# Optimization experiments

Hardware: AMD Instinct MI355X
Metric: run time of the kernel (lower is better)

The kernel has to match this reference:

```python
import jax, jax.numpy as jnp
import numpy as np

NUM_HEAD = 2
KR = 3          # kernel_range = [3, 3]
SHIFT = 1
N_P = KR * KR   # 9 taps
PAD = (KR // 2) * SHIFT  # 1
OFFSETS = [(i, j) for i in (-(KR // 2), 0, KR // 2) if True for j in ()]  # placeholder, real list below
OFFSETS = [(i, j) for i in range(-(KR // 2), KR // 2 + 1) for j in range(-(KR // 2), KR // 2 + 1)]


def _conv3x3(x, w, b):
    # x: [B,H,W,Cin], w: [3,3,Cin,Cout] -> SAME conv + bias
    y = jax.lax.conv_general_dilated(
        x, w, window_strides=(1, 1), padding='SAME',
        dimension_numbers=('NHWC', 'HWIO', 'NHWC'))
    return y + b


def setup_inputs() -> dict:
    key = jax.random.key(0)
    B, H, W, D = 4, 128, 128, 64
    ks = jax.random.split(key, 10)
    sc = 0.05  # small init like glorot
    return {
        'x': jax.random.normal(ks[0], (B, H, W, D), jnp.float32),
        # 1x1 conv kernels stored as matrices (equiv. to (1,1,Cin,Cout))
        'K_P': jax.random.normal(ks[1], (D, D * N_P), jnp.float32) * sc,
        'V_P': jax.random.normal(ks[2], (D, D * N_P), jnp.float32) * sc,
        'Q_P': jax.random.normal(ks[3], (D, D), jnp.float32) * sc,
        'ff1_kernel': jax.random.normal(ks[4], (D, D), jnp.float32) * sc,
        'ff1_bias': jax.random.normal(ks[5], (D,), jnp.float32) * sc,
        'ff2_kernel': jax.random.normal(ks[6], (3, 3, D, 2 * D), jnp.float32) * sc,
        'ff2_bias': jax.random.normal(ks[7], (2 * D,), jnp.float32) * sc,
        'ff3_kernel': jax.random.normal(ks[8], (3, 3, 2 * D, D), jnp.float32) * sc,
        'ff3_bias': jax.random.normal(ks[9], (D,), jnp.float32) * sc,
    }


def reference(x, K_P, V_P, Q_P, ff1_kernel, ff1_bias, ff2_kernel, ff2_bias,
              ff3_kernel, ff3_bias):
    B, H, W, D = x.shape
    hd = D // NUM_HEAD

    # 1x1 projections; K/V produce N_P channel chunks, one per tap
    x_k = jnp.einsum('bhwd,de->bhwe', x, K_P).reshape(B, H, W, N_P, D)
    x_v = jnp.einsum('bhwd,de->bhwe', x, V_P).reshape(B, H, W, N_P, D)
    x_q = jnp.einsum('bhwd,de->bhwe', x, Q_P)

    pad5 = ((0, 0), (PAD, PAD), (PAD, PAD), (0, 0), (0, 0))
    k_pad = jnp.pad(x_k, pad5)
    v_pad = jnp.pad(x_v, pad5)

    # tap t uses channel chunk t at spatial offset OFFSETS[t]*SHIFT
    def taps(padded):
        return jnp.stack(
            [padded[:, PAD + i * SHIFT:PAD + i * SHIFT + H,
                    PAD + j * SHIFT:PAD + j * SHIFT + W, t, :]
             for t, (i, j) in enumerate(OFFSETS)], axis=3)  # [B,H,W,N_P,D]

    k_taps = taps(k_pad)
    v_taps = taps(v_pad)

    # validity mask (padded taps get score 0 before softmax, as in original)
    m_pad = jnp.pad(jnp.ones((B, H, W), x.dtype), ((0, 0), (PAD, PAD), (PAD, PAD)))
    mask = jnp.stack(
        [m_pad[:, PAD + i * SHIFT:PAD + i * SHIFT + H,
               PAD + j * SHIFT:PAD + j * SHIFT + W]
         for (i, j) in OFFSETS], axis=3)  # [B,H,W,N_P]

    kh = k_taps.reshape(B, H, W, N_P, NUM_HEAD, hd)
    vh = v_taps.reshape(B, H, W, N_P, NUM_HEAD, hd)
    qh = x_q.reshape(B, H, W, NUM_HEAD, hd)

    # scores per head over taps; masked-multiply then /3, as in original
    scores = jnp.einsum('bhwtnc,bhwnc->bhwnt', kh, qh)
    scores = scores * mask[:, :, :, None, :] / 3.0
    alpha = jax.nn.softmax(scores, axis=-1)  # over taps
    attn = jnp.einsum('bhwnt,bhwtnc->bhwnc', alpha, vh).reshape(B, H, W, D)

    # FFN: 1x1 conv -> relu -> 3x3 conv -> relu -> 3x3 conv -> relu
    t = jax.nn.relu(jnp.einsum('bhwd,de->bhwe', attn, ff1_kernel) + ff1_bias)
    t = jax.nn.relu(_conv3x3(t, ff2_kernel, ff2_bias))
    t = jax.nn.relu(_conv3x3(t, ff3_kernel, ff3_bias))
    return t
```

## Files before the change

### kernel.cpp

```cpp
#include <hip/hip_runtime.h>


typedef _Float16 half8 __attribute__((ext_vector_type(8)));
typedef float f32x4 __attribute__((ext_vector_type(4)));

#define PLANE 524288

__device__ __forceinline__ f32x4 mfma16(half8 a, half8 b, f32x4 c) {
  return __builtin_amdgcn_mfma_f32_16x16x32_f16(a, b, c, 0, 0, 0);
}
__device__ __forceinline__ half8 ldfrag(const _Float16* p) { return *(const half8*)p; }
__device__ __forceinline__ half8 zfrag() { half8 z = {}; return z; }

__device__ __forceinline__ int xcd_swz(int n, int chunk) {
  return (n & 7) * chunk + (n >> 3);
}

__device__ __forceinline__ void gload_lds16(const _Float16* g, _Float16* l) {
  __builtin_amdgcn_global_load_lds(
      (const __attribute__((address_space(1))) void*)g,
      (__attribute__((address_space(3))) void*)l, 16, 0, 0);
}

__global__ __launch_bounds__(256) void prep(
    const float* __restrict__ x, const float* __restrict__ Kp,
    const float* __restrict__ Vp, const float* __restrict__ Qp,
    const float* __restrict__ W1, const float* __restrict__ F2,
    const float* __restrict__ F3, _Float16* __restrict__ xh,
    _Float16* __restrict__ out) {
  if (blockIdx.x < 2048) {
    const int b = xcd_swz(blockIdx.x, 256);
    const int t = threadIdx.x;
    const int px = b * 32 + (t >> 3);
    const int oct = t & 7;
    const float4* s = (const float4*)(x + (size_t)px * 64 + oct * 8);
    float4 a = s[0], b4 = s[1];
    half8 h = { (_Float16)a.x, (_Float16)a.y, (_Float16)a.z, (_Float16)a.w,
                (_Float16)b4.x, (_Float16)b4.y, (_Float16)b4.z, (_Float16)b4.w };
    *(half8*)(xh + (size_t)oct * PLANE + (size_t)px * 8) = h;
    return;
  }
  int e = (blockIdx.x - 2048) * 256 + threadIdx.x;
  int j = e & 7, l = (e >> 3) & 63, f = e >> 9;
  int l15 = l & 15, q8 = (l >> 4) * 8;
  float v;
  if (f < 8)        { int mb = f >> 1, kb = f & 1;
                      v = Qp[(kb*32 + q8 + j) * 64 + mb*16 + l15]; }
  else if (f < 80)  { int g = f - 8, t = g >> 3, mb = (g >> 1) & 3, kb = g & 1;
                      v = Kp[(kb*32 + q8 + j) * 576 + t*64 + mb*16 + l15]; }
  else if (f < 152) { int g = f - 80, t = g >> 3, kb = (g >> 2) & 1, nb = g & 3;
                      v = Vp[(kb*32 + q8 + j) * 576 + t*64 + nb*16 + l15]; }
  else if (f < 160) { int g = f - 152, kb = g >> 2, nb = g & 3;
                      v = W1[(kb*32 + q8 + j) * 64 + nb*16 + l15]; }
  else if (f < 304) { int g = f - 160, t = g >> 4, kb = (g >> 3) & 1, nb = g & 7;
                      v = F2[(t*64 + kb*32 + q8 + j) * 128 + nb*16 + l15]; }
  else              { int g = f - 304, t = g >> 4, kb = (g >> 2) & 3, nb = g & 3;
                      v = F3[(t*128 + kb*32 + q8 + j) * 64 + nb*16 + l15]; }
  out[e] = (_Float16)v;
}

__global__ __launch_bounds__(1024, 4) void attn_ff1(
    const _Float16* __restrict__ xh, const _Float16* __restrict__ wf,
    const float* __restrict__ f1b, _Float16* __restrict__ t1g) {
  extern __shared__ _Float16 smem[];
  const int lane = threadIdx.x & 63, wid = threadIdx.x >> 6;
  const int l15 = lane & 15, q8 = (lane >> 4) * 8;
  const int bid = xcd_swz(blockIdx.x, 32);
  const int row = bid * 2 + (wid >> 3);
  const int rw = wid & 7;
  const int p0 = row * 128 + rw * 16;
  const int h = row & 127;
  const int w0 = rw * 16;
  const int oct0 = lane >> 4;
  float* dent = (float*)(smem + 77824) + wid * 32;

  {
    for (int i = 0; i < 10; ++i) {
      int f = wid * 10 + i;
      if (f < 152)
        gload_lds16(wf + 4096 + (size_t)f * 512 + lane * 8,
                    smem + (size_t)f * 512);
    }
  }

  half8 ax0, ax1;
  {
    const size_t px = (size_t)(p0 + l15);
    ax0 = ldfrag(xh + (size_t)oct0 * PLANE + px * 8);
    ax1 = ldfrag(xh + (size_t)(oct0 + 4) * PLANE + px * 8);
  }
  f32x4 qT[4];
#pragma unroll
  for (int cb = 0; cb < 4; ++cb) {
    half8 aq0 = ldfrag(wf + (cb * 2 + 0) * 512 + lane * 8);
    half8 aq1 = ldfrag(wf + (cb * 2 + 1) * 512 + lane * 8);
    f32x4 c = {};
    c = mfma16(aq0, ax0, c);
    c = mfma16(aq1, ax1, c);
    qT[cb] = c;
  }

  auto load_tap = [&](int t, half8& x0, half8& x1) {
    const int dh = t / 3 - 1, dw = t % 3 - 1;
    const bool rk = (unsigned)(h + dh) < 128u;
    const bool cv = rk && ((unsigned)(w0 + l15 + dw) < 128u);
    const size_t px = (size_t)(p0 + l15 + dh * 128 + dw);
    x0 = cv ? ldfrag(xh + (size_t)oct0 * PLANE + px * 8) : zfrag();
    x1 = cv ? ldfrag(xh + (size_t)(oct0 + 4) * PLANE + px * 8) : zfrag();
  };

  float den0 = 0.f, den1 = 0.f;
  auto score_tap = [&](int t, half8& x0, half8& x1, float& e0, float& e1) {
    const int dh = t / 3 - 1;
    const bool rowok = (unsigned)(h + dh) < 128u;
    half8 kf[8];
    if (rowok) {
#pragma unroll
      for (int f = 0; f < 8; ++f)
        kf[f] = ldfrag(smem + (t * 8 + f) * 512 + lane * 8);
    }
    float pa = 0.f, pb = 0.f;
    if (rowok) {
#pragma unroll
      for (int cb = 0; cb < 4; ++cb) {
        f32x4 c = {};
        c = mfma16(kf[cb * 2 + 0], x0, c);
        c = mfma16(kf[cb * 2 + 1], x1, c);
        float d = qT[cb].x * c.x + qT[cb].y * c.y
                + qT[cb].z * c.z + qT[cb].w * c.w;
        if (cb < 2) pa += d; else pb += d;
      }
      pa += __shfl_xor(pa, 16, 64); pa += __shfl_xor(pa, 32, 64);
      pb += __shfl_xor(pb, 16, 64); pb += __shfl_xor(pb, 32, 64);
    }
    e0 = __expf(pa * (1.f / 3.f));
    e1 = __expf(pb * (1.f / 3.f));
    den0 += e0; den1 += e1;
  };

  half8 q0[3], q1[3];
  load_tap(0, q0[0], q1[0]);
  load_tap(1, q0[1], q1[1]);

  __syncthreads();

  float e0c, e1c;
  score_tap(0, q0[0], q1[0], e0c, e1c);

  const _Float16* BVl = smem + 36864;
  f32x4 at[4];
#pragma unroll
  for (int nb = 0; nb < 4; ++nb) at[nb] = f32x4{};

#pragma unroll
  for (int t = 0; t < 9; ++t) {
    if (t + 2 < 9) load_tap(t + 2, q0[(t + 2) % 3], q1[(t + 2) % 3]);
    const bool rowok = (unsigned)(h + (t / 3 - 1)) < 128u;
    if (rowok) {
      half8 vf[8];
#pragma unroll
      for (int f = 0; f < 8; ++f)
        vf[f] = ldfrag(BVl + (t * 8 + f) * 512 + lane * 8);
      _Float16 h0 = (_Float16)e0c, h1 = (_Float16)e1c;
      half8 b0 = {h0, h0, h0, h0, h0, h0, h0, h0};
      half8 b1 = {h1, h1, h1, h1, h1, h1, h1, h1};
      half8 s00 = q0[t % 3] * b0, s01 = q1[t % 3] * b0;
      half8 s10 = q0[t % 3] * b1, s11 = q1[t % 3] * b1;
#pragma unroll
      for (int nb = 0; nb < 2; ++nb) {
        at[nb]     = mfma16(s00, vf[0 * 4 + nb],     at[nb]);
        at[nb]     = mfma16(s01, vf[1 * 4 + nb],     at[nb]);
        at[nb + 2] = mfma16(s10, vf[0 * 4 + nb + 2], at[nb + 2]);
        at[nb + 2] = mfma16(s11, vf[1 * 4 + nb + 2], at[nb + 2]);
      }
    }
    if (t < 8) {
      float e0n, e1n;
      score_tap(t + 1, q0[(t + 1) % 3], q1[(t + 1) % 3], e0n, e1n);
      e0c = e0n; e1c = e1n;
    }
  }

  dent[0 * 16 + l15] = den0;
  dent[1 * 16 + l15] = den1;
  f32x4 iv[2];
#pragma unroll
  for (int hd = 0; hd < 2; ++hd) {
    f32x4 dv = *(const f32x4*)(dent + hd * 16 + (lane >> 4) * 4);
    iv[hd] = f32x4{1.f / dv.x, 1.f / dv.y, 1.f / dv.z, 1.f / dv.w};
  }

  __syncthreads();
  _Float16* myt = smem + wid * 1152;
#pragma unroll
  for (int nb = 0; nb < 4; ++nb) {
    const int hd = nb >> 1;
#pragma unroll
    for (int r = 0; r < 4; ++r)
      myt[((lane >> 4) * 4 + r) * 72 + nb * 16 + l15] =
          (_Float16)(at[nb][r] * iv[hd][r]);
  }
  const _Float16* B1l = smem + 73728;
  const int pxl = lane >> 2;
  const int co0 = lane & 3;
  half8 aa0 = ldfrag(myt + l15 * 72 + q8);
  half8 aa1 = ldfrag(myt + l15 * 72 + 32 + q8);
#pragma unroll
  for (int nb = 0; nb < 4; ++nb) {
    f32x4 c = {};
    c = mfma16(aa0, ldfrag(B1l + (0 * 4 + nb) * 512 + lane * 8), c);
    c = mfma16(aa1, ldfrag(B1l + (1 * 4 + nb) * 512 + lane * 8), c);
    float bv = f1b[nb * 16 + l15];
#pragma unroll
    for (int r = 0; r < 4; ++r)
      myt[((lane >> 4) * 4 + r) * 72 + nb * 16 + l15] =
          (_Float16)fmaxf(c[r] + bv, 0.f);
  }
  const size_t pxg = (size_t)(p0 + pxl);
  half8 h0 = ldfrag(myt + pxl * 72 + co0 * 8);
  half8 h1 = ldfrag(myt + pxl * 72 + (co0 + 4) * 8);
  *(half8*)(t1g + (size_t)co0 * PLANE + pxg * 8) = h0;
  *(half8*)(t1g + (size_t)(co0 + 4) * PLANE + pxg * 8) = h1;
}

template <int KB, int NBL, int COUT, int DEPTH>
__global__ __launch_bounds__(512, 4) void conv3x3(
    const _Float16* __restrict__ in, const _Float16* __restrict__ wfrag,
    const float* __restrict__ bias, void* __restrict__ outp, int out_fp32) {
  extern __shared__ _Float16 smem[];
  constexpr int NS = DEPTH + 1;
  const int lane = threadIdx.x & 63, wid = threadIdx.x >> 6;
  const int l15 = lane & 15;
  const int bid = xcd_swz(blockIdx.x, 64);
  const int nh = bid & 1;
  const int pairIdx = bid >> 1;
  const int row = pairIdx * 2 + (wid >> 2);
  const int rw = wid & 3;
  const int p0 = row * 128 + rw * 32;
  const int h = row & 127;
  const int w0 = rw * 32;
  const int NBF = COUT / 16;
  const int oct0 = lane >> 4;

  {
    for (int s = 0; s < 9; ++s) {
      int f = wid * 9 + s;
      int t = f >> 3, r = f & 7, kb = r / NBL, i = r % NBL;
      const _Float16* g = wfrag + (size_t)((t * KB + kb) * NBF + nh * NBL + i) * 512;
      gload_lds16(g + lane * 8, smem + f * 512);
    }
  }

  f32x4 acc[2][NBL];
#pragma unroll
  for (int m = 0; m < 2; ++m)
#pragma unroll
    for (int nb = 0; nb < NBL; ++nb) acc[m][nb] = f32x4{};

  auto load_conv = [&](int t, half8 (&dst)[2][KB]) {
    const int dh = t / 3 - 1, dw = t % 3 - 1;
    const bool rk = (unsigned)(h + dh) < 128u;
#pragma unroll
    for (int m = 0; m < 2; ++m) {
      const bool cv = rk && ((unsigned)(w0 + m * 16 + l15 + dw) < 128u);
      const size_t px = (size_t)(p0 + m * 16 + l15 + dh * 128 + dw);
#pragma unroll
      for (int kb = 0; kb < KB; ++kb)
        dst[m][kb] = cv ? ldfrag(in + (size_t)(kb * 4 + oct0) * PLANE + px * 8) : zfrag();
    }
  };

  half8 aq[NS][2][KB];
#pragma unroll
  for (int d = 0; d < DEPTH; ++d) load_conv(d, aq[d]);

  __syncthreads();

#pragma unroll
  for (int t = 0; t < 9; ++t) {
    if (t + DEPTH < 9) load_conv(t + DEPTH, aq[(t + DEPTH) % NS]);
    const bool rowok = (unsigned)(h + (t / 3 - 1)) < 128u;
    if (rowok) {
#pragma unroll
      for (int nb = 0; nb < NBL; ++nb) {
#pragma unroll
        for (int kb = 0; kb < KB; ++kb) {
          half8 b = ldfrag(smem + (size_t)((t * KB + kb) * NBL + nb) * 512 + lane * 8);
          acc[0][nb] = mfma16(aq[t % NS][0][kb], b, acc[0][nb]);
          acc[1][nb] = mfma16(aq[t % NS][1][kb], b, acc[1][nb]);
        }
      }
    }
  }

  if (out_fp32) {
#pragma unroll
    for (int m = 0; m < 2; ++m)
#pragma unroll
      for (int nb = 0; nb < NBL; ++nb) {
        const int ch = nh * NBL * 16 + nb * 16 + l15;
        float bv = bias[ch];
#pragma unroll
        for (int r = 0; r < 4; ++r) {
          float v = fmaxf(acc[m][nb][r] + bv, 0.f);
          size_t px = (size_t)(p0 + m * 16 + (lane >> 4) * 4 + r);
          ((float*)outp)[px * COUT + ch] = v;
        }
      }
  } else {
    __syncthreads();
    _Float16* T = smem + wid * 1152;
    const int pxl = lane >> 2, co0 = lane & 3;
#pragma unroll
    for (int m = 0; m < 2; ++m) {
#pragma unroll
      for (int nb = 0; nb < NBL; ++nb) {
        const int chl = nb * 16 + l15;
        float bv = bias[nh * NBL * 16 + chl];
#pragma unroll
        for (int r = 0; r < 4; ++r)
          T[((lane >> 4) * 4 + r) * 72 + chl] =
              (_Float16)fmaxf(acc[m][nb][r] + bv, 0.f);
      }
      const size_t pxg = (size_t)(p0 + m * 16 + pxl);
      half8 h0 = ldfrag(T + pxl * 72 + co0 * 8);
      half8 h1 = ldfrag(T + pxl * 72 + (co0 + 4) * 8);
      *(half8*)((_Float16*)outp + (size_t)(nh * 8 + co0) * PLANE + pxg * 8) = h0;
      *(half8*)((_Float16*)outp + (size_t)(nh * 8 + co0 + 4) * PLANE + pxg * 8) = h1;
    }
  }
}

__global__ __launch_bounds__(512, 4) void conv3b(
    const _Float16* __restrict__ in, const _Float16* __restrict__ wfrag,
    const float* __restrict__ bias, float* __restrict__ outp) {
  extern __shared__ _Float16 smem[];
  const int lane = threadIdx.x & 63, wid = threadIdx.x >> 6;
  const int l15 = lane & 15;
  const int bid = xcd_swz(blockIdx.x, 64);
  const int nh = bid & 1;
  const int pairIdx = bid >> 1;
  const int row = pairIdx * 2 + (wid >> 2);
  const int rw = wid & 3;
  const int p0 = row * 128 + rw * 32;
  const int h = row & 127;
  const int w0 = rw * 32;
  const int oct0 = lane >> 4;
  const int KB = 4, NBL = 2, NBF = 4, COUT = 64;

  {
    for (int s = 0; s < 9; ++s) {
      int f = wid * 9 + s;
      int t = f >> 3, r = f & 7, kb = r / NBL, i = r % NBL;
      const _Float16* g = wfrag + (size_t)((t * KB + kb) * NBF + nh * NBL + i) * 512;
      gload_lds16(g + lane * 8, smem + f * 512);
    }
  }

  f32x4 acc[2][2];
#pragma unroll
  for (int m = 0; m < 2; ++m)
#pragma unroll
    for (int nb = 0; nb < 2; ++nb) acc[m][nb] = f32x4{};

#pragma unroll
  for (int p = 0; p < 2; ++p) {
    auto load_half = [&](int t, half8 (&dst)[2][2]) {
      const int dh = t / 3 - 1, dw = t % 3 - 1;
      const bool rk = (unsigned)(h + dh) < 128u;
#pragma unroll
      for (int m = 0; m < 2; ++m) {
        const bool cv = rk && ((unsigned)(w0 + m * 16 + l15 + dw) < 128u);
        const size_t px = (size_t)(p0 + m * 16 + l15 + dh * 128 + dw);
#pragma unroll
        for (int kbl = 0; kbl < 2; ++kbl)
          dst[m][kbl] = cv
              ? ldfrag(in + (size_t)((2 * p + kbl) * 4 + oct0) * PLANE + px * 8)
              : zfrag();
      }
    };

    half8 aq[3][2][2];
    load_half(0, aq[0]);
    load_half(1, aq[1]);
    if (p == 0) __syncthreads();

#pragma unroll
    for (int t = 0; t < 9; ++t) {
      if (t + 2 < 9) load_half(t + 2, aq[(t + 2) % 3]);
      const bool rowok = (unsigned)(h + (t / 3 - 1)) < 128u;
      if (rowok) {
#pragma unroll
        for (int nb = 0; nb < 2; ++nb) {
#pragma unroll
          for (int kbl = 0; kbl < 2; ++kbl) {
            half8 b = ldfrag(smem +
                (size_t)((t * KB + 2 * p + kbl) * NBL + nb) * 512 + lane * 8);
            acc[0][nb] = mfma16(aq[t % 3][0][kbl], b, acc[0][nb]);
            acc[1][nb] = mfma16(aq[t % 3][1][kbl], b, acc[1][nb]);
          }
        }
      }
    }
  }

#pragma unroll
  for (int m = 0; m < 2; ++m)
#pragma unroll
    for (int nb = 0; nb < 2; ++nb) {
      const int ch = nh * 32 + nb * 16 + l15;
      float bv = bias[ch];
#pragma unroll
      for (int r = 0; r < 4; ++r) {
        float v = fmaxf(acc[m][nb][r] + bv, 0.f);
        size_t px = (size_t)(p0 + m * 16 + (lane >> 4) * 4 + r);
        outp[px * COUT + ch] = v;
      }
    }
}

extern "C" void kernel_launch(void* const* d_in, const int* in_sizes, int n_in,
                              void* d_out, int out_size, void* d_ws, size_t ws_size,
                              hipStream_t stream) {
  (void)in_sizes; (void)n_in; (void)out_size; (void)ws_size;
  const float* x   = (const float*)d_in[0];
  const float* Kp  = (const float*)d_in[1];
  const float* Vp  = (const float*)d_in[2];
  const float* Qp  = (const float*)d_in[3];
  const float* f1w = (const float*)d_in[4];
  const float* f1b = (const float*)d_in[5];
  const float* f2w = (const float*)d_in[6];
  const float* f2b = (const float*)d_in[7];
  const float* f3w = (const float*)d_in[8];
  const float* f3b = (const float*)d_in[9];

  _Float16* xh  = (_Float16*)d_ws;
  _Float16* wf  = xh + 4194304;
  _Float16* t1g = wf + 229376;
  _Float16* t2g = t1g + 4194304;
  float* outp = (float*)d_out;

  (void)hipFuncSetAttribute((const void*)attn_ff1,
      hipFuncAttributeMaxDynamicSharedMemorySize, 157696);
  (void)hipFuncSetAttribute((const void*)conv3x3<2, 4, 128, 3>,
      hipFuncAttributeMaxDynamicSharedMemorySize, 73728);
  (void)hipFuncSetAttribute((const void*)conv3b,
      hipFuncAttributeMaxDynamicSharedMemorySize, 73728);

  prep<<<2944, 256, 0, stream>>>(x, Kp, Vp, Qp, f1w, f2w, f3w, xh, wf);
  attn_ff1<<<256, 1024, 157696, stream>>>(xh, wf, f1b, t1g);
  conv3x3<2, 4, 128, 3><<<512, 512, 73728, stream>>>(t1g, wf + 81920, f2b, t2g, 0);
  conv3b<<<512, 512, 73728, stream>>>(t2g, wf + 155648, f3b, outp);
}
```

Baseline: 135.0 us.

## Fuse fp32-to-fp16 input conversion into attention kernel and raise MFMA priority

Removes the separate pass that converted x to planar fp16 in the prep kernel. The attention kernel now reads fp32 x directly, converts each tap on the fly, and keeps a two-deep ring of raw float4 loads in registers. It also wraps the MFMA inner loops in all three compute kernels with s_setprio to favour matrix issue. The trade-off is twice as many bytes per tap read by the attention kernel and higher register pressure from raw fp32 staging, in exchange for dropping a full write and read of a converted copy of x.

```diff
diff --git a/kernel.cpp b/kernel.cpp
--- a/kernel.cpp
+++ b/kernel.cpp
@@ -11,6 +11,10 @@
 }
 __device__ __forceinline__ half8 ldfrag(const _Float16* p) { return *(const half8*)p; }
 __device__ __forceinline__ half8 zfrag() { half8 z = {}; return z; }
+__device__ __forceinline__ half8 cvt8(float4 a, float4 b) {
+  return half8{(_Float16)a.x, (_Float16)a.y, (_Float16)a.z, (_Float16)a.w,
+               (_Float16)b.x, (_Float16)b.y, (_Float16)b.z, (_Float16)b.w};
+}
 
 __device__ __forceinline__ int xcd_swz(int n, int chunk) {
   return (n & 7) * chunk + (n >> 3);
@@ -23,24 +27,11 @@
 }
 
 __global__ __launch_bounds__(256) void prep(
-    const float* __restrict__ x, const float* __restrict__ Kp,
-    const float* __restrict__ Vp, const float* __restrict__ Qp,
-    const float* __restrict__ W1, const float* __restrict__ F2,
-    const float* __restrict__ F3, _Float16* __restrict__ xh,
+    const float* __restrict__ Kp, const float* __restrict__ Vp,
+    const float* __restrict__ Qp, const float* __restrict__ W1,
+    const float* __restrict__ F2, const float* __restrict__ F3,
     _Float16* __restrict__ out) {
-  if (blockIdx.x < 2048) {
-    const int b = xcd_swz(blockIdx.x, 256);
-    const int t = threadIdx.x;
-    const int px = b * 32 + (t >> 3);
-    const int oct = t & 7;
-    const float4* s = (const float4*)(x + (size_t)px * 64 + oct * 8);
-    float4 a = s[0], b4 = s[1];
-    half8 h = { (_Float16)a.x, (_Float16)a.y, (_Float16)a.z, (_Float16)a.w,
-                (_Float16)b4.x, (_Float16)b4.y, (_Float16)b4.z, (_Float16)b4.w };
-    *(half8*)(xh + (size_t)oct * PLANE + (size_t)px * 8) = h;
-    return;
-  }
-  int e = (blockIdx.x - 2048) * 256 + threadIdx.x;
+  int e = blockIdx.x * 256 + threadIdx.x;
   int j = e & 7, l = (e >> 3) & 63, f = e >> 9;
   int l15 = l & 15, q8 = (l >> 4) * 8;
   float v;
@@ -60,7 +51,7 @@
 }
 
 __global__ __launch_bounds__(1024, 4) void attn_ff1(
-    const _Float16* __restrict__ xh, const _Float16* __restrict__ wf,
+    const float* __restrict__ x, const _Float16* __restrict__ wf,
     const float* __restrict__ f1b, _Float16* __restrict__ t1g) {
   extern __shared__ _Float16 smem[];
   const int lane = threadIdx.x & 63, wid = threadIdx.x >> 6;
@@ -85,9 +76,11 @@
 
   half8 ax0, ax1;
   {
-    const size_t px = (size_t)(p0 + l15);
-    ax0 = ldfrag(xh + (size_t)oct0 * PLANE + px * 8);
-    ax1 = ldfrag(xh + (size_t)(oct0 + 4) * PLANE + px * 8);
+    const float* base = x + (size_t)(p0 + l15) * 64;
+    const float4* s0 = (const float4*)(base + oct0 * 8);
+    const float4* s1 = (const float4*)(base + (oct0 + 4) * 8);
+    ax0 = cvt8(s0[0], s0[1]);
+    ax1 = cvt8(s1[0], s1[1]);
   }
   f32x4 qT[4];
 #pragma unroll
@@ -100,19 +93,28 @@
     qT[cb] = c;
   }
 
-  auto load_tap = [&](int t, half8& x0, half8& x1) {
+  struct Raw { float4 a0, b0, a1, b1; };
+  Raw rq[2];
+  auto load_raw = [&](int t, Raw& r) {
     const int dh = t / 3 - 1, dw = t % 3 - 1;
     const bool rk = (unsigned)(h + dh) < 128u;
     const bool cv = rk && ((unsigned)(w0 + l15 + dw) < 128u);
-    const size_t px = (size_t)(p0 + l15 + dh * 128 + dw);
-    x0 = cv ? ldfrag(xh + (size_t)oct0 * PLANE + px * 8) : zfrag();
-    x1 = cv ? ldfrag(xh + (size_t)(oct0 + 4) * PLANE + px * 8) : zfrag();
+    if (cv) {
+      const float* base = x + (size_t)(p0 + l15 + dh * 128 + dw) * 64;
+      const float4* s0 = (const float4*)(base + oct0 * 8);
+      const float4* s1 = (const float4*)(base + (oct0 + 4) * 8);
+      r.a0 = s0[0]; r.b0 = s0[1]; r.a1 = s1[0]; r.b1 = s1[1];
+    } else {
+      float4 z = {};
+      r.a0 = z; r.b0 = z; r.a1 = z; r.b1 = z;
+    }
   };
 
   float den0 = 0.f, den1 = 0.f;
-  auto score_tap = [&](int t, half8& x0, half8& x1, float& e0, float& e1) {
+  auto score_tap = [&](int t, const Raw& r, float& e0, float& e1) {
     const int dh = t / 3 - 1;
     const bool rowok = (unsigned)(h + dh) < 128u;
+    half8 x0 = cvt8(r.a0, r.b0), x1 = cvt8(r.a1, r.b1);
     half8 kf[8];
     if (rowok) {
 #pragma unroll
@@ -138,14 +140,13 @@
     den0 += e0; den1 += e1;
   };
 
-  half8 q0[3], q1[3];
-  load_tap(0, q0[0], q1[0]);
-  load_tap(1, q0[1], q1[1]);
+  load_raw(0, rq[0]);
+  load_raw(1, rq[1]);
 
   __syncthreads();
 
   float e0c, e1c;
-  score_tap(0, q0[0], q1[0], e0c, e1c);
+  score_tap(0, rq[0], e0c, e1c);
 
   const _Float16* BVl = smem + 36864;
   f32x4 at[4];
@@ -154,8 +155,10 @@
 
 #pragma unroll
   for (int t = 0; t < 9; ++t) {
-    if (t + 2 < 9) load_tap(t + 2, q0[(t + 2) % 3], q1[(t + 2) % 3]);
     const bool rowok = (unsigned)(h + (t / 3 - 1)) < 128u;
+    half8 x0 = cvt8(rq[t & 1].a0, rq[t & 1].b0);
+    half8 x1 = cvt8(rq[t & 1].a1, rq[t & 1].b1);
+    if (t + 2 < 9) load_raw(t + 2, rq[t & 1]);
     if (rowok) {
       half8 vf[8];
 #pragma unroll
@@ -164,8 +167,9 @@
       _Float16 h0 = (_Float16)e0c, h1 = (_Float16)e1c;
       half8 b0 = {h0, h0, h0, h0, h0, h0, h0, h0};
       half8 b1 = {h1, h1, h1, h1, h1, h1, h1, h1};
-      half8 s00 = q0[t % 3] * b0, s01 = q1[t % 3] * b0;
-      half8 s10 = q0[t % 3] * b1, s11 = q1[t % 3] * b1;
+      half8 s00 = x0 * b0, s01 = x1 * b0;
+      half8 s10 = x0 * b1, s11 = x1 * b1;
+      __builtin_amdgcn_s_setprio(1);
 #pragma unroll
       for (int nb = 0; nb < 2; ++nb) {
         at[nb]     = mfma16(s00, vf[0 * 4 + nb],     at[nb]);
@@ -173,10 +177,11 @@
         at[nb + 2] = mfma16(s10, vf[0 * 4 + nb + 2], at[nb + 2]);
         at[nb + 2] = mfma16(s11, vf[1 * 4 + nb + 2], at[nb + 2]);
       }
+      __builtin_amdgcn_s_setprio(0);
     }
     if (t < 8) {
       float e0n, e1n;
-      score_tap(t + 1, q0[(t + 1) % 3], q1[(t + 1) % 3], e0n, e1n);
+      score_tap(t + 1, rq[(t + 1) & 1], e0n, e1n);
       e0c = e0n; e1c = e1n;
     }
   }
@@ -281,6 +286,7 @@
     if (t + DEPTH < 9) load_conv(t + DEPTH, aq[(t + DEPTH) % NS]);
     const bool rowok = (unsigned)(h + (t / 3 - 1)) < 128u;
     if (rowok) {
+      __builtin_amdgcn_s_setprio(1);
 #pragma unroll
       for (int nb = 0; nb < NBL; ++nb) {
 #pragma unroll
@@ -290,6 +296,7 @@
           acc[1][nb] = mfma16(aq[t % NS][1][kb], b, acc[1][nb]);
         }
       }
+      __builtin_amdgcn_s_setprio(0);
     }
   }
 
@@ -390,6 +397,7 @@
       if (t + 2 < 9) load_half(t + 2, aq[(t + 2) % 3]);
       const bool rowok = (unsigned)(h + (t / 3 - 1)) < 128u;
       if (rowok) {
+        __builtin_amdgcn_s_setprio(1);
 #pragma unroll
         for (int nb = 0; nb < 2; ++nb) {
 #pragma unroll
@@ -400,6 +408,7 @@
             acc[1][nb] = mfma16(aq[t % 3][1][kbl], b, acc[1][nb]);
           }
         }
+        __builtin_amdgcn_s_setprio(0);
       }
     }
   }
@@ -434,8 +443,7 @@
   const float* f3w = (const float*)d_in[8];
   const float* f3b = (const float*)d_in[9];
 
-  _Float16* xh  = (_Float16*)d_ws;
-  _Float16* wf  = xh + 4194304;
+  _Float16* wf  = (_Float16*)d_ws;
   _Float16* t1g = wf + 229376;
   _Float16* t2g = t1g + 4194304;
   float* outp = (float*)d_out;
@@ -447,8 +455,8 @@
   (void)hipFuncSetAttribute((const void*)conv3b,
       hipFuncAttributeMaxDynamicSharedMemorySize, 73728);
 
-  prep<<<2944, 256, 0, stream>>>(x, Kp, Vp, Qp, f1w, f2w, f3w, xh, wf);
-  attn_ff1<<<256, 1024, 157696, stream>>>(xh, wf, f1b, t1g);
+  prep<<<896, 256, 0, stream>>>(Kp, Vp, Qp, f1w, f2w, f3w, wf);
+  attn_ff1<<<256, 1024, 157696, stream>>>(x, wf, f1b, t1g);
   conv3x3<2, 4, 128, 3><<<512, 512, 73728, stream>>>(t1g, wf + 81920, f2b, t2g, 0);
   conv3b<<<512, 512, 73728, stream>>>(t2g, wf + 155648, f3b, outp);
 }
```

Result: slower. 146.3 us (+8.3%).

## Widen conv3x3 warp tiles to 64 pixels and reuse template for final conv

Applied to the files above, without the earlier changes.

The conv3x3 kernel gains an M template parameter so each wave computes 64 pixels (4 M-tiles) instead of 32, which halves the block count and reuses each LDS weight fragment across more MFMAs. The dedicated conv3b kernel is removed and the final conv uses the generic template with fp32 output. The cost is more registers per wave (launch bounds relaxed to 2 blocks per SM) and only 256 blocks, which lowers occupancy and parallelism.

```diff
diff --git a/kernel.cpp b/kernel.cpp
--- a/kernel.cpp
+++ b/kernel.cpp
@@ -223,22 +223,22 @@
   *(half8*)(t1g + (size_t)(co0 + 4) * PLANE + pxg * 8) = h1;
 }
 
-template <int KB, int NBL, int COUT, int DEPTH>
-__global__ __launch_bounds__(512, 4) void conv3x3(
+template <int KB, int NBL, int COUT, int DEPTH, int M>
+__global__ __launch_bounds__(512, 2) void conv3x3(
     const _Float16* __restrict__ in, const _Float16* __restrict__ wfrag,
     const float* __restrict__ bias, void* __restrict__ outp, int out_fp32) {
   extern __shared__ _Float16 smem[];
   constexpr int NS = DEPTH + 1;
   const int lane = threadIdx.x & 63, wid = threadIdx.x >> 6;
   const int l15 = lane & 15;
-  const int bid = xcd_swz(blockIdx.x, 64);
+  const int bid = xcd_swz(blockIdx.x, 32);
   const int nh = bid & 1;
-  const int pairIdx = bid >> 1;
-  const int row = pairIdx * 2 + (wid >> 2);
-  const int rw = wid & 3;
-  const int p0 = row * 128 + rw * 32;
+  const int rg = bid >> 1;
+  const int row = rg * 4 + (wid >> 1);
+  const int rw = wid & 1;
+  const int p0 = row * 128 + rw * 64;
   const int h = row & 127;
-  const int w0 = rw * 32;
+  const int w0 = rw * 64;
   const int NBF = COUT / 16;
   const int oct0 = lane >> 4;
 
@@ -251,17 +251,17 @@
     }
   }
 
-  f32x4 acc[2][NBL];
-#pragma unroll
-  for (int m = 0; m < 2; ++m)
+  f32x4 acc[M][NBL];
+#pragma unroll
+  for (int m = 0; m < M; ++m)
 #pragma unroll
     for (int nb = 0; nb < NBL; ++nb) acc[m][nb] = f32x4{};
 
-  auto load_conv = [&](int t, half8 (&dst)[2][KB]) {
+  auto load_conv = [&](int t, half8 (&dst)[M][KB]) {
     const int dh = t / 3 - 1, dw = t % 3 - 1;
     const bool rk = (unsigned)(h + dh) < 128u;
 #pragma unroll
-    for (int m = 0; m < 2; ++m) {
+    for (int m = 0; m < M; ++m) {
       const bool cv = rk && ((unsigned)(w0 + m * 16 + l15 + dw) < 128u);
       const size_t px = (size_t)(p0 + m * 16 + l15 + dh * 128 + dw);
 #pragma unroll
@@ -270,7 +270,7 @@
     }
   };
 
-  half8 aq[NS][2][KB];
+  half8 aq[NS][M][KB];
 #pragma unroll
   for (int d = 0; d < DEPTH; ++d) load_conv(d, aq[d]);
 
@@ -286,8 +286,9 @@
 #pragma unroll
         for (int kb = 0; kb < KB; ++kb) {
           half8 b = ldfrag(smem + (size_t)((t * KB + kb) * NBL + nb) * 512 + lane * 8);
-          acc[0][nb] = mfma16(aq[t % NS][0][kb], b, acc[0][nb]);
-          acc[1][nb] = mfma16(aq[t % NS][1][kb], b, acc[1][nb]);
+#pragma unroll
+          for (int m = 0; m < M; ++m)
+            acc[m][nb] = mfma16(aq[t % NS][m][kb], b, acc[m][nb]);
         }
       }
     }
@@ -295,7 +296,7 @@
 
   if (out_fp32) {
 #pragma unroll
-    for (int m = 0; m < 2; ++m)
+    for (int m = 0; m < M; ++m)
 #pragma unroll
       for (int nb = 0; nb < NBL; ++nb) {
         const int ch = nh * NBL * 16 + nb * 16 + l15;
@@ -312,7 +313,7 @@
     _Float16* T = smem + wid * 1152;
     const int pxl = lane >> 2, co0 = lane & 3;
 #pragma unroll
-    for (int m = 0; m < 2; ++m) {
+    for (int m = 0; m < M; ++m) {
 #pragma unroll
       for (int nb = 0; nb < NBL; ++nb) {
         const int chl = nb * 16 + l15;
@@ -329,94 +330,6 @@
       *(half8*)((_Float16*)outp + (size_t)(nh * 8 + co0 + 4) * PLANE + pxg * 8) = h1;
     }
   }
-}
-
-__global__ __launch_bounds__(512, 4) void conv3b(
-    const _Float16* __restrict__ in, const _Float16* __restrict__ wfrag,
-    const float* __restrict__ bias, float* __restrict__ outp) {
-  extern __shared__ _Float16 smem[];
-  const int lane = threadIdx.x & 63, wid = threadIdx.x >> 6;
-  const int l15 = lane & 15;
-  const int bid = xcd_swz(blockIdx.x, 64);
-  const int nh = bid & 1;
-  const int pairIdx = bid >> 1;
-  const int row = pairIdx * 2 + (wid >> 2);
-  const int rw = wid & 3;
-  const int p0 = row * 128 + rw * 32;
-  const int h = row & 127;
-  const int w0 = rw * 32;
-  const int oct0 = lane >> 4;
-  const int KB = 4, NBL = 2, NBF = 4, COUT = 64;
-
-  {
-    for (int s = 0; s < 9; ++s) {
-      int f = wid * 9 + s;
-      int t = f >> 3, r = f & 7, kb = r / NBL, i = r % NBL;
-      const _Float16* g = wfrag + (size_t)((t * KB + kb) * NBF + nh * NBL + i) * 512;
-      gload_lds16(g + lane * 8, smem + f * 512);
-    }
-  }
-
-  f32x4 acc[2][2];
-#pragma unroll
-  for (int m = 0; m < 2; ++m)
-#pragma unroll
-    for (int nb = 0; nb < 2; ++nb) acc[m][nb] = f32x4{};
-
-#pragma unroll
-  for (int p = 0; p < 2; ++p) {
-    auto load_half = [&](int t, half8 (&dst)[2][2]) {
-      const int dh = t / 3 - 1, dw = t % 3 - 1;
-      const bool rk = (unsigned)(h + dh) < 128u;
-#pragma unroll
-      for (int m = 0; m < 2; ++m) {
-        const bool cv = rk && ((unsigned)(w0 + m * 16 + l15 + dw) < 128u);
-        const size_t px = (size_t)(p0 + m * 16 + l15 + dh * 128 + dw);
-#pragma unroll
-        for (int kbl = 0; kbl < 2; ++kbl)
-          dst[m][kbl] = cv
-              ? ldfrag(in + (size_t)((2 * p + kbl) * 4 + oct0) * PLANE + px * 8)
-              : zfrag();
-      }
-    };
-
-    half8 aq[3][2][2];
-    load_half(0, aq[0]);
-    load_half(1, aq[1]);
-    if (p == 0) __syncthreads();
-
-#pragma unroll
-    for (int t = 0; t < 9; ++t) {
-      if (t + 2 < 9) load_half(t + 2, aq[(t + 2) % 3]);
-      const bool rowok = (unsigned)(h + (t / 3 - 1)) < 128u;
-      if (rowok) {
-#pragma unroll
-        for (int nb = 0; nb < 2; ++nb) {
-#pragma unroll
-          for (int kbl = 0; kbl < 2; ++kbl) {
-            half8 b = ldfrag(smem +
-                (size_t)((t * KB + 2 * p + kbl) * NBL + nb) * 512 + lane * 8);
-            acc[0][nb] = mfma16(aq[t % 3][0][kbl], b, acc[0][nb]);
-            acc[1][nb] = mfma16(aq[t % 3][1][kbl], b, acc[1][nb]);
-          }
-        }
-      }
-    }
-  }
-
-#pragma unroll
-  for (int m = 0; m < 2; ++m)
-#pragma unroll
-    for (int nb = 0; nb < 2; ++nb) {
-      const int ch = nh * 32 + nb * 16 + l15;
-      float bv = bias[ch];
-#pragma unroll
-      for (int r = 0; r < 4; ++r) {
-        float v = fmaxf(acc[m][nb][r] + bv, 0.f);
-        size_t px = (size_t)(p0 + m * 16 + (lane >> 4) * 4 + r);
-        outp[px * COUT + ch] = v;
-      }
-    }
 }
 
 extern "C" void kernel_launch(void* const* d_in, const int* in_sizes, int n_in,
@@ -442,13 +355,13 @@
 
   (void)hipFuncSetAttribute((const void*)attn_ff1,
       hipFuncAttributeMaxDynamicSharedMemorySize, 157696);
-  (void)hipFuncSetAttribute((const void*)conv3x3<2, 4, 128, 3>,
+  (void)hipFuncSetAttribute((const void*)conv3x3<2, 4, 128, 3, 4>,
       hipFuncAttributeMaxDynamicSharedMemorySize, 73728);
-  (void)hipFuncSetAttribute((const void*)conv3b,
+  (void)hipFuncSetAttribute((const void*)conv3x3<4, 2, 64, 2, 4>,
       hipFuncAttributeMaxDynamicSharedMemorySize, 73728);
 
   prep<<<2944, 256, 0, stream>>>(x, Kp, Vp, Qp, f1w, f2w, f3w, xh, wf);
   attn_ff1<<<256, 1024, 157696, stream>>>(xh, wf, f1b, t1g);
-  conv3x3<2, 4, 128, 3><<<512, 512, 73728, stream>>>(t1g, wf + 81920, f2b, t2g, 0);
-  conv3b<<<512, 512, 73728, stream>>>(t2g, wf + 155648, f3b, outp);
-}
+  conv3x3<2, 4, 128, 3, 4><<<256, 512, 73728, stream>>>(t1g, wf + 81920, f2b, t2g, 0);
+  conv3x3<4, 2, 64, 2, 4><<<256, 512, 73728, stream>>>(t2g, wf + 155648, f3b, outp, 1);
+}
```

Result: slower. 145.1 us (+7.4%).
